# Kernel optimization log

Measured on AMD Instinct MI355X. Metric: run time of the kernel, lower is better.

The kernel has to match this reference:

```python
import jax, jax.numpy as jnp
import numpy as np

NHEAD = 16


def setup_inputs() -> dict:
    key = jax.random.key(0)
    ks = jax.random.split(key, 6)
    S, B, D = 2048, 2, 1024
    std = float(np.sqrt(6.0 / (D + D)))  # xavier_uniform bound
    inp = {
        "query": jax.random.normal(ks[0], (S, B, D), jnp.float32),
        "key": jax.random.normal(ks[1], (S, B, D), jnp.float32),
        "value": jax.random.normal(ks[2], (S, B, D), jnp.float32),
        "Wq": jax.random.uniform(ks[3], (D, D), jnp.float32, -std, std),
        "bq": jnp.ones((D,), jnp.float32),
        "Wk": jax.random.uniform(ks[4], (D, D), jnp.float32, -std, std),
        "bk": jnp.ones((D,), jnp.float32),
        "Wv": jax.random.uniform(ks[5], (D, D), jnp.float32, -std, std),
        "bv": jnp.ones((D,), jnp.float32),
    }
    return inp


def reference(query, key, value, Wq, bq, Wk, bk, Wv, bv):
    S, B, D = query.shape
    h = NHEAD
    d = D // h
    scale = jnp.asarray(d ** 0.5, query.dtype)
    # projections (nn.Linear: x @ W^T + b)
    q = (query @ Wq.T + bq).reshape(S, B, h, d)
    k = (key @ Wk.T + bk).reshape(S, B, h, d)
    v = (value @ Wv.T + bv).reshape(S, B, h, d)
    # batch_first=False path: scores [b,h,i,j], softmax over j, then AV
    scores = jnp.einsum('ibhd,jbhd->bhij', q, k) / scale
    attn = jax.nn.softmax(scores, axis=-1)
    out = jnp.einsum('bhij,jbhd->ibhd', attn, v).reshape(S, B, D)
    return out
```

## Files before the change

kernel.cpp:

```cpp
#include <hip/hip_runtime.h>
#include <hip/hip_bf16.h>

#define S_LEN 2048
#define BATCH 2
#define DMODEL 1024
#define NHEAD 16
#define HDIM 64
#define MTOT (S_LEN * BATCH)
#define QKV_ELEMS ((size_t)MTOT * DMODEL)
#define XOFF (3 * QKV_ELEMS)
#define WOFF (XOFF + 3 * QKV_ELEMS)
#define WSEG ((size_t)DMODEL * DMODEL)

typedef __bf16 bf16x8 __attribute__((ext_vector_type(8)));
typedef unsigned short u16x8 __attribute__((ext_vector_type(8)));
typedef float f32x4 __attribute__((ext_vector_type(4)));
typedef float f32x16 __attribute__((ext_vector_type(16)));
typedef unsigned int u32x4 __attribute__((ext_vector_type(4)));

__device__ __forceinline__ unsigned short f2bf(float f) {
    unsigned int u = __float_as_uint(f);
    u += 0x7FFFu + ((u >> 16) & 1u);
    return (unsigned short)(u >> 16);
}

__device__ __forceinline__ unsigned int pack2(float lo, float hi) {
    __hip_bfloat162 h = __float22bfloat162_rn(make_float2(lo, hi));
    unsigned int r;
    __builtin_memcpy(&r, &h, 4);
    return r;
}

__device__ __forceinline__ void gload_lds16(const void* g, void* l) {
    __builtin_amdgcn_global_load_lds(
        (const __attribute__((address_space(1))) unsigned int*)g,
        (__attribute__((address_space(3))) unsigned int*)l, 16, 0, 0);
}

__global__ __launch_bounds__(256) void cvt_kernel(
        const float* __restrict__ Xq, const float* __restrict__ Xk,
        const float* __restrict__ Xv, const float* __restrict__ Wq,
        const float* __restrict__ Wk, const float* __restrict__ Wv,
        unsigned short* __restrict__ ws)
{
    const int seg = blockIdx.y;
    const float* src;
    unsigned short* dst;
    int n4;
    if (seg < 3) {
        src = (seg == 0) ? Xq : (seg == 1) ? Xk : Xv;
        dst = ws + XOFF + (size_t)seg * QKV_ELEMS;
        n4  = (int)(QKV_ELEMS / 4);
    } else {
        const int s = seg - 3;
        src = (s == 0) ? Wq : (s == 1) ? Wk : Wv;
        dst = ws + WOFF + (size_t)s * WSEG;
        n4  = (int)(WSEG / 4);
    }
    const int stride = gridDim.x * blockDim.x;
    for (int i = blockIdx.x * blockDim.x + threadIdx.x; i < n4; i += stride) {
        const float4 v = ((const float4*)src)[i];
        uint2 o;
        o.x = pack2(v.x, v.y);
        o.y = pack2(v.z, v.w);
        ((uint2*)dst)[i] = o;
    }
}

#define PBM 128
#define PBN 128
#define PBK 32
#define QSCALE 0.18033688011112042f

__global__ __launch_bounds__(256, 3) void proj_kernel(
        const unsigned short* __restrict__ wsin,
        const float* __restrict__ bq, const float* __restrict__ bk,
        const float* __restrict__ bv, unsigned short* __restrict__ wsout)
{
    const int work = (blockIdx.x & 7) * 96 + (blockIdx.x >> 3);
    const int t    = work >> 8;
    const int rem  = work & 255;
    const int m0   = (rem >> 3) * PBM;
    const int n0   = (rem & 7) * PBN;

    const unsigned short* X = wsin + XOFF + (size_t)t * QKV_ELEMS;
    const unsigned short* W = wsin + WOFF + (size_t)t * WSEG;
    const float* bias = (t == 0) ? bq : (t == 1) ? bk : bv;
    unsigned short* out = wsout + (size_t)t * QKV_ELEMS;
    const float scale = (t == 0) ? QSCALE : 1.0f;

    __shared__ __align__(16) unsigned short Abuf[2][PBM * PBK];
    __shared__ __align__(16) unsigned short Bbuf[2][PBN * PBK];

    const int tid  = threadIdx.x;
    const int wave = tid >> 6;
    const int lane = tid & 63;
    const int lrow = lane & 15;
    const int lg   = lane >> 4;
    const int wr = (wave >> 1) * 64;
    const int wc = (wave & 1) * 64;

    f32x4 acc[4][4];
#pragma unroll
    for (int i = 0; i < 4; ++i)
#pragma unroll
        for (int j = 0; j < 4; ++j)
            acc[i][j] = (f32x4){0.f, 0.f, 0.f, 0.f};

    const int srow_ = tid >> 2;
    const int sc_   = tid & 3;
    const int gsw = (lg ^ (lrow & 3)) * 8;

#pragma unroll
    for (int i0 = 0; i0 < 2; ++i0) {
        const int row = i0 * 64 + srow_;
        const int c   = sc_ ^ (row & 3);
        gload_lds16(X + (size_t)(m0 + row) * DMODEL + c * 8, &Abuf[0][i0 * 2048 + tid * 8]);
        gload_lds16(W + (size_t)(n0 + row) * DMODEL + c * 8, &Bbuf[0][i0 * 2048 + tid * 8]);
    }
    __syncthreads();

    int cur = 0;
    for (int k0 = 0; k0 < DMODEL; k0 += PBK) {
        if (k0 + PBK < DMODEL) {
#pragma unroll
            for (int i0 = 0; i0 < 2; ++i0) {
                const int row = i0 * 64 + srow_;
                const int c   = sc_ ^ (row & 3);
                gload_lds16(X + (size_t)(m0 + row) * DMODEL + k0 + PBK + c * 8,
                            &Abuf[cur ^ 1][i0 * 2048 + tid * 8]);
                gload_lds16(W + (size_t)(n0 + row) * DMODEL + k0 + PBK + c * 8,
                            &Bbuf[cur ^ 1][i0 * 2048 + tid * 8]);
            }
        }

        bf16x8 af[4], bw[4];
#pragma unroll
        for (int i = 0; i < 4; ++i) {
            af[i] = *(const bf16x8*)&Abuf[cur][(wr + i * 16 + lrow) * PBK + gsw];
            bw[i] = *(const bf16x8*)&Bbuf[cur][(wc + i * 16 + lrow) * PBK + gsw];
        }
        __builtin_amdgcn_s_setprio(1);
#pragma unroll
        for (int i = 0; i < 4; ++i)
#pragma unroll
            for (int j = 0; j < 4; ++j)
                acc[i][j] = __builtin_amdgcn_mfma_f32_16x16x32_bf16(af[i], bw[j], acc[i][j], 0, 0, 0);
        __builtin_amdgcn_s_setprio(0);

        __syncthreads();
        cur ^= 1;
    }

#pragma unroll
    for (int j = 0; j < 4; ++j) {
        const int n  = n0 + wc + j * 16 + lrow;
        const float bv_ = bias[n];
        const int h  = n >> 6;
        const int dd = n & 63;
#pragma unroll
        for (int i = 0; i < 4; ++i) {
#pragma unroll
            for (int r = 0; r < 4; ++r) {
                const int m = m0 + wr + i * 16 + lg * 4 + r;
                const int s = m >> 1;
                const int b = m & 1;
                const float v = (acc[i][j][r] + bv_) * scale;
                size_t idx;
                if (t == 2)
                    idx = ((size_t)((b * NHEAD + h) * HDIM + dd)) * S_LEN + s;
                else
                    idx = ((size_t)((b * NHEAD + h) * S_LEN + s)) * HDIM + dd;
                out[idx] = f2bf(v);
            }
        }
    }
}

#define NP 32

__global__ __launch_bounds__(512, 4) void attn_kernel(
        const unsigned short* __restrict__ ws, float* __restrict__ out)
{
    const unsigned short* Qw = ws;
    const unsigned short* Kw = ws + QKV_ELEMS;
    const unsigned short* Vw = ws + 2 * QKV_ELEMS;

    const int bid = blockIdx.x;
    const int idx = bid >> 3;
    const int bh  = (bid & 7) * 4 + (idx >> 4);
    const int q0  = (idx & 15) * 128;

    __shared__ __align__(16) unsigned short SMEM[24576];
    unsigned short* Kb = SMEM;
    unsigned short* Vb = SMEM + 8192;
    unsigned int*   Pb = (unsigned int*)(SMEM + 16384);

    const int tid  = threadIdx.x;
    const int wave = tid >> 6;
    const int lane = tid & 63;
    const int l31  = lane & 31;
    const int half = lane >> 5;
    const int qsub = wave >> 1;
    const int pw   = wave & 1;

    const size_t base = (size_t)bh * S_LEN * HDIM;
    const int qrow = q0 + qsub * 32 + l31;

    bf16x8 qf[4];
#pragma unroll
    for (int c = 0; c < 4; ++c)
        qf[c] = *(const bf16x8*)(Qw + base + (size_t)qrow * HDIM + c * 16 + half * 8);

    bf16x8 ones;
    {
        u16x8 o;
#pragma unroll
        for (int e = 0; e < 8; ++e) o[e] = 0x3F80;
        ones = __builtin_bit_cast(bf16x8, o);
    }

    f32x16 Od0, Od1, Lacc;
#pragma unroll
    for (int i = 0; i < 16; ++i) { Od0[i] = 0.f; Od1[i] = 0.f; Lacc[i] = 0.f; }
    float mrun = -__builtin_inff();

    unsigned int* PuW = Pb + wave * 512;

    const int stile = tid >> 8;
    const int t256  = tid & 255;
    const int ksrow = t256 >> 3;
    const int ksg   = (t256 & 7) ^ (ksrow & 7);
    const int vrow  = t256 >> 2;
    const int vsg   = (t256 & 3) ^ ((vrow >> 1) & 3);

    int gk[4], gv[2];
#pragma unroll
    for (int c = 0; c < 4; ++c) gk[c] = ((c * 2 + half) ^ (l31 & 7)) * 8;
#pragma unroll
    for (int c = 0; c < 2; ++c) gv[c] = ((c * 2 + half) ^ ((l31 >> 1) & 3)) * 8;

    {
        const int tt = stile;
        gload_lds16(Kw + base + (size_t)(tt * 32 + ksrow) * HDIM + ksg * 8, &Kb[(tt & 3) * 2048 + t256 * 8]);
        gload_lds16(Vw + base + (size_t)vrow * S_LEN + tt * 32 + vsg * 8,   &Vb[(tt & 3) * 2048 + t256 * 8]);
    }
    __syncthreads();

    for (int p = 0; p < NP; ++p) {
        if (p < NP - 1) {
            const int tt = 2 * p + 2 + stile;
            gload_lds16(Kw + base + (size_t)(tt * 32 + ksrow) * HDIM + ksg * 8, &Kb[(tt & 3) * 2048 + t256 * 8]);
            gload_lds16(Vw + base + (size_t)vrow * S_LEN + tt * 32 + vsg * 8,   &Vb[(tt & 3) * 2048 + t256 * 8]);
        }

        const int tm = 2 * p + pw;
        const unsigned short* Klds = &Kb[(tm & 3) * 2048];
        const unsigned short* Vlds = &Vb[(tm & 3) * 2048];

        f32x16 S;
#pragma unroll
        for (int i = 0; i < 16; ++i) S[i] = 0.f;
        __builtin_amdgcn_s_setprio(1);
#pragma unroll
        for (int c = 0; c < 4; ++c) {
            const bf16x8 ka = *(const bf16x8*)&Klds[l31 * 64 + gk[c]];
            S = __builtin_amdgcn_mfma_f32_32x32x16_bf16(ka, qf[c], S, 0, 0, 0);
        }
        __builtin_amdgcn_s_setprio(0);

        float m8_[8];
#pragma unroll
        for (int i = 0; i < 8; ++i) m8_[i] = fmaxf(S[i], S[i + 8]);
        const float t0 = fmaxf(fmaxf(m8_[0], m8_[1]), m8_[2]);
        const float t1 = fmaxf(fmaxf(m8_[3], m8_[4]), m8_[5]);
        const float t2 = fmaxf(fmaxf(m8_[6], m8_[7]), t0);
        float mx = fmaxf(t1, t2);
        mx = fmaxf(mx, __shfl_xor(mx, 32, 64));

        if (!__all(mx - mrun <= 8.0f)) {
            const float mnew = fmaxf(mrun, mx);
            const float ex   = exp2f(mrun - mnew);
            mrun = mnew;
            Od0 *= ex;
            Od1 *= ex;
            Lacc *= ex;
        }

#pragma unroll
        for (int i = 0; i < 16; ++i) S[i] = exp2f(S[i] - mrun);

#pragma unroll
        for (int u = 0; u < 4; ++u) {
            uint2 two;
            two.x = pack2(S[4 * u],     S[4 * u + 1]);
            two.y = pack2(S[4 * u + 2], S[4 * u + 3]);
            *(uint2*)&PuW[(2 * u + half) * 64 + l31 * 2] = two;
        }
        __asm__ volatile("" ::: "memory");

        __builtin_amdgcn_s_setprio(1);
#pragma unroll
        for (int c = 0; c < 2; ++c) {
            const int row0 = 4 * c + 2 * half;
            const uint2 a = *(const uint2*)&PuW[row0 * 64 + l31 * 2];
            const uint2 b = *(const uint2*)&PuW[(row0 + 1) * 64 + l31 * 2];
            u32x4 pu; pu[0] = a.x; pu[1] = a.y; pu[2] = b.x; pu[3] = b.y;
            const bf16x8 pb = __builtin_bit_cast(bf16x8, pu);
            const bf16x8 va0 = *(const bf16x8*)&Vlds[l31 * 32 + gv[c]];
            const bf16x8 va1 = *(const bf16x8*)&Vlds[(32 + l31) * 32 + gv[c]];
            Od0  = __builtin_amdgcn_mfma_f32_32x32x16_bf16(va0,  pb, Od0,  0, 0, 0);
            Od1  = __builtin_amdgcn_mfma_f32_32x32x16_bf16(va1,  pb, Od1,  0, 0, 0);
            Lacc = __builtin_amdgcn_mfma_f32_32x32x16_bf16(ones, pb, Lacc, 0, 0, 0);
        }
        __builtin_amdgcn_s_setprio(0);

        __syncthreads();
    }

    float* mrg = (float*)SMEM;
    float* reg = mrg + qsub * 2176;
    if (pw) {
        reg[lane]      = mrun;
        reg[64 + lane] = Lacc[0];
#pragma unroll
        for (int i = 0; i < 16; ++i) {
            reg[128 + i * 64 + lane]        = Od0[i];
            reg[128 + (16 + i) * 64 + lane] = Od1[i];
        }
    }
    __syncthreads();
    if (!pw) {
        const float mb = reg[lane];
        const float lb = reg[64 + lane];
        const float ms = fmaxf(mrun, mb);
        const float sa = exp2f(mrun - ms);
        const float sb = exp2f(mb - ms);
        const float linv = 1.0f / (Lacc[0] * sa + lb * sb);

        const int bb = bh >> 4;
        const int hh = bh & 15;
        float* op = out + (size_t)qrow * (BATCH * DMODEL) + bb * DMODEL + hh * HDIM;
#pragma unroll
        for (int gg = 0; gg < 4; ++gg) {
            const int d0 = gg * 8 + half * 4;
            float4 v0, v1;
            v0.x = (Od0[gg * 4 + 0] * sa + reg[128 + (gg * 4 + 0) * 64 + lane] * sb) * linv;
            v0.y = (Od0[gg * 4 + 1] * sa + reg[128 + (gg * 4 + 1) * 64 + lane] * sb) * linv;
            v0.z = (Od0[gg * 4 + 2] * sa + reg[128 + (gg * 4 + 2) * 64 + lane] * sb) * linv;
            v0.w = (Od0[gg * 4 + 3] * sa + reg[128 + (gg * 4 + 3) * 64 + lane] * sb) * linv;
            v1.x = (Od1[gg * 4 + 0] * sa + reg[128 + (16 + gg * 4 + 0) * 64 + lane] * sb) * linv;
            v1.y = (Od1[gg * 4 + 1] * sa + reg[128 + (16 + gg * 4 + 1) * 64 + lane] * sb) * linv;
            v1.z = (Od1[gg * 4 + 2] * sa + reg[128 + (16 + gg * 4 + 2) * 64 + lane] * sb) * linv;
            v1.w = (Od1[gg * 4 + 3] * sa + reg[128 + (16 + gg * 4 + 3) * 64 + lane] * sb) * linv;
            *(float4*)(op + d0)      = v0;
            *(float4*)(op + 32 + d0) = v1;
        }
    }
}

extern "C" void kernel_launch(void* const* d_in, const int* in_sizes, int n_in,
                              void* d_out, int out_size, void* d_ws, size_t ws_size,
                              hipStream_t stream) {
    const float* q  = (const float*)d_in[0];
    const float* k  = (const float*)d_in[1];
    const float* v  = (const float*)d_in[2];
    const float* Wq = (const float*)d_in[3];
    const float* bq = (const float*)d_in[4];
    const float* Wk = (const float*)d_in[5];
    const float* bk = (const float*)d_in[6];
    const float* Wv = (const float*)d_in[7];
    const float* bv = (const float*)d_in[8];
    unsigned short* ws = (unsigned short*)d_ws;
    float* out = (float*)d_out;

    cvt_kernel<<<dim3(1024, 6), dim3(256), 0, stream>>>(q, k, v, Wq, Wk, Wv, ws);
    proj_kernel<<<dim3(768), dim3(256), 0, stream>>>(ws, bq, bk, bv, ws);
    attn_kernel<<<dim3(512), dim3(512), 0, stream>>>(ws, out);
}
```

Measured before the change: 133.6 us.

## Software-pipeline attention loop: overlap next QK^T MFMA with current softmax and PV

Restructures the flash-attention main loop into a software pipeline. The QK^T MFMAs for the next tile and the PV MFMAs for the previous tile are issued around the softmax of the current tile. The K/V LDS ring grows from 4 to 6 slots so a prefetch two periods ahead does not overwrite tiles still in use, and __syncthreads becomes an explicit vmcnt wait plus barrier. The aim is to hide the exp and softmax latency behind matrix-core work, at the cost of more LDS (which may lower occupancy) and more live registers. Only Lacc[0] is rescaled now, which relies on only element 0 being read later.

```diff
diff --git a/kernel.cpp b/kernel.cpp
--- a/kernel.cpp
+++ b/kernel.cpp
@@ -191,10 +191,10 @@
     const int bh  = (bid & 7) * 4 + (idx >> 4);
     const int q0  = (idx & 15) * 128;
 
-    __shared__ __align__(16) unsigned short SMEM[24576];
+    __shared__ __align__(16) unsigned short SMEM[32768];
     unsigned short* Kb = SMEM;
-    unsigned short* Vb = SMEM + 8192;
-    unsigned int*   Pb = (unsigned int*)(SMEM + 16384);
+    unsigned short* Vb = SMEM + 12288;
+    unsigned int*   Pb = (unsigned int*)(SMEM + 24576);
 
     const int tid  = threadIdx.x;
     const int wave = tid >> 6;
@@ -225,6 +225,8 @@
     for (int i = 0; i < 16; ++i) { Od0[i] = 0.f; Od1[i] = 0.f; Lacc[i] = 0.f; }
     float mrun = -__builtin_inff();
 
+    bf16x8 pb[2], va[4];
+
     unsigned int* PuW = Pb + wave * 512;
 
     const int stile = tid >> 8;
@@ -240,82 +242,128 @@
 #pragma unroll
     for (int c = 0; c < 2; ++c) gv[c] = ((c * 2 + half) ^ ((l31 >> 1) & 3)) * 8;
 
+#pragma unroll
+    for (int q = 0; q < 2; ++q) {
+        const int tt = 2 * q + stile;
+        gload_lds16(Kw + base + (size_t)(tt * 32 + ksrow) * HDIM + ksg * 8, &Kb[tt * 2048 + t256 * 8]);
+        gload_lds16(Vw + base + (size_t)vrow * S_LEN + tt * 32 + vsg * 8,   &Vb[tt * 2048 + t256 * 8]);
+    }
+    asm volatile("s_waitcnt vmcnt(0)" ::: "memory");
+    __builtin_amdgcn_s_barrier();
+
+    f32x16 Sa, Sb;
+
     {
-        const int tt = stile;
-        gload_lds16(Kw + base + (size_t)(tt * 32 + ksrow) * HDIM + ksg * 8, &Kb[(tt & 3) * 2048 + t256 * 8]);
-        gload_lds16(Vw + base + (size_t)vrow * S_LEN + tt * 32 + vsg * 8,   &Vb[(tt & 3) * 2048 + t256 * 8]);
-    }
-    __syncthreads();
-
-    for (int p = 0; p < NP; ++p) {
-        if (p < NP - 1) {
-            const int tt = 2 * p + 2 + stile;
-            gload_lds16(Kw + base + (size_t)(tt * 32 + ksrow) * HDIM + ksg * 8, &Kb[(tt & 3) * 2048 + t256 * 8]);
-            gload_lds16(Vw + base + (size_t)vrow * S_LEN + tt * 32 + vsg * 8,   &Vb[(tt & 3) * 2048 + t256 * 8]);
-        }
-
-        const int tm = 2 * p + pw;
-        const unsigned short* Klds = &Kb[(tm & 3) * 2048];
-        const unsigned short* Vlds = &Vb[(tm & 3) * 2048];
-
-        f32x16 S;
-#pragma unroll
-        for (int i = 0; i < 16; ++i) S[i] = 0.f;
+#pragma unroll
+        for (int i = 0; i < 16; ++i) Sa[i] = 0.f;
+        const unsigned short* Kl = &Kb[pw * 2048];
         __builtin_amdgcn_s_setprio(1);
 #pragma unroll
         for (int c = 0; c < 4; ++c) {
-            const bf16x8 ka = *(const bf16x8*)&Klds[l31 * 64 + gk[c]];
-            S = __builtin_amdgcn_mfma_f32_32x32x16_bf16(ka, qf[c], S, 0, 0, 0);
+            const bf16x8 ka = *(const bf16x8*)&Kl[l31 * 64 + gk[c]];
+            Sa = __builtin_amdgcn_mfma_f32_32x32x16_bf16(ka, qf[c], Sa, 0, 0, 0);
         }
         __builtin_amdgcn_s_setprio(0);
-
-        float m8_[8];
-#pragma unroll
-        for (int i = 0; i < 8; ++i) m8_[i] = fmaxf(S[i], S[i + 8]);
-        const float t0 = fmaxf(fmaxf(m8_[0], m8_[1]), m8_[2]);
-        const float t1 = fmaxf(fmaxf(m8_[3], m8_[4]), m8_[5]);
-        const float t2 = fmaxf(fmaxf(m8_[6], m8_[7]), t0);
-        float mx = fmaxf(t1, t2);
-        mx = fmaxf(mx, __shfl_xor(mx, 32, 64));
-
-        if (!__all(mx - mrun <= 8.0f)) {
-            const float mnew = fmaxf(mrun, mx);
-            const float ex   = exp2f(mrun - mnew);
-            mrun = mnew;
-            Od0 *= ex;
-            Od1 *= ex;
-            Lacc *= ex;
-        }
-
-#pragma unroll
-        for (int i = 0; i < 16; ++i) S[i] = exp2f(S[i] - mrun);
-
-#pragma unroll
-        for (int u = 0; u < 4; ++u) {
-            uint2 two;
-            two.x = pack2(S[4 * u],     S[4 * u + 1]);
-            two.y = pack2(S[4 * u + 2], S[4 * u + 3]);
-            *(uint2*)&PuW[(2 * u + half) * 64 + l31 * 2] = two;
-        }
-        __asm__ volatile("" ::: "memory");
-
+    }
+
+    int qsb = 2;
+    int csb = 0;
+
+    auto period = [&](f32x16& SCUR, f32x16& SNXT, const int p) {
+        if (p + 2 < NP) {
+            int ssb = qsb + 2; if (ssb >= 6) ssb -= 6;
+            const int tt = 2 * (p + 2) + stile;
+            gload_lds16(Kw + base + (size_t)(tt * 32 + ksrow) * HDIM + ksg * 8, &Kb[(ssb + stile) * 2048 + t256 * 8]);
+            gload_lds16(Vw + base + (size_t)vrow * S_LEN + tt * 32 + vsg * 8,   &Vb[(ssb + stile) * 2048 + t256 * 8]);
+        }
+        if (p + 1 < NP) {
+#pragma unroll
+            for (int i = 0; i < 16; ++i) SNXT[i] = 0.f;
+            const unsigned short* Kl = &Kb[(qsb + pw) * 2048];
+            __builtin_amdgcn_s_setprio(1);
+#pragma unroll
+            for (int c = 0; c < 4; ++c) {
+                const bf16x8 ka = *(const bf16x8*)&Kl[l31 * 64 + gk[c]];
+                SNXT = __builtin_amdgcn_mfma_f32_32x32x16_bf16(ka, qf[c], SNXT, 0, 0, 0);
+            }
+            __builtin_amdgcn_s_setprio(0);
+        }
+        if (p >= 1) {
+            __builtin_amdgcn_s_setprio(1);
+#pragma unroll
+            for (int c = 0; c < 2; ++c) {
+                Od0  = __builtin_amdgcn_mfma_f32_32x32x16_bf16(va[2 * c],     pb[c], Od0,  0, 0, 0);
+                Od1  = __builtin_amdgcn_mfma_f32_32x32x16_bf16(va[2 * c + 1], pb[c], Od1,  0, 0, 0);
+                Lacc = __builtin_amdgcn_mfma_f32_32x32x16_bf16(ones,          pb[c], Lacc, 0, 0, 0);
+            }
+            __builtin_amdgcn_s_setprio(0);
+        }
+        {
+            float m8_[8];
+#pragma unroll
+            for (int i = 0; i < 8; ++i) m8_[i] = fmaxf(SCUR[i], SCUR[i + 8]);
+            const float t0 = fmaxf(fmaxf(m8_[0], m8_[1]), m8_[2]);
+            const float t1 = fmaxf(fmaxf(m8_[3], m8_[4]), m8_[5]);
+            const float t2 = fmaxf(fmaxf(m8_[6], m8_[7]), t0);
+            float mx = fmaxf(t1, t2);
+            mx = fmaxf(mx, __shfl_xor(mx, 32, 64));
+
+            if (!__all(mx - mrun <= 8.0f)) {
+                const float mnew = fmaxf(mrun, mx);
+                const float ex   = exp2f(mrun - mnew);
+                mrun = mnew;
+                Od0 *= ex;
+                Od1 *= ex;
+                Lacc[0] *= ex;
+            }
+#pragma unroll
+            for (int i = 0; i < 16; ++i) SCUR[i] = exp2f(SCUR[i] - mrun);
+
+#pragma unroll
+            for (int u = 0; u < 4; ++u) {
+                uint2 two;
+                two.x = pack2(SCUR[4 * u],     SCUR[4 * u + 1]);
+                two.y = pack2(SCUR[4 * u + 2], SCUR[4 * u + 3]);
+                *(uint2*)&PuW[(2 * u + half) * 64 + l31 * 2] = two;
+            }
+            __asm__ volatile("" ::: "memory");
+        }
+        {
+#pragma unroll
+            for (int c = 0; c < 2; ++c) {
+                const int row0 = 4 * c + 2 * half;
+                const uint2 a = *(const uint2*)&PuW[row0 * 64 + l31 * 2];
+                const uint2 b = *(const uint2*)&PuW[(row0 + 1) * 64 + l31 * 2];
+                u32x4 pu; pu[0] = a.x; pu[1] = a.y; pu[2] = b.x; pu[3] = b.y;
+                pb[c] = __builtin_bit_cast(bf16x8, pu);
+            }
+            const unsigned short* Vl = &Vb[(csb + pw) * 2048];
+#pragma unroll
+            for (int c = 0; c < 2; ++c) {
+                va[2 * c]     = *(const bf16x8*)&Vl[l31 * 32 + gv[c]];
+                va[2 * c + 1] = *(const bf16x8*)&Vl[(32 + l31) * 32 + gv[c]];
+            }
+        }
+        asm volatile("s_waitcnt vmcnt(0)" ::: "memory");
+        __builtin_amdgcn_s_barrier();
+        qsb = (qsb >= 4) ? qsb - 4 : qsb + 2;
+        csb = (csb >= 4) ? csb - 4 : csb + 2;
+    };
+
+    for (int it = 0; it < NP / 2; ++it) {
+        period(Sa, Sb, 2 * it);
+        period(Sb, Sa, 2 * it + 1);
+    }
+
+    {
         __builtin_amdgcn_s_setprio(1);
 #pragma unroll
         for (int c = 0; c < 2; ++c) {
-            const int row0 = 4 * c + 2 * half;
-            const uint2 a = *(const uint2*)&PuW[row0 * 64 + l31 * 2];
-            const uint2 b = *(const uint2*)&PuW[(row0 + 1) * 64 + l31 * 2];
-            u32x4 pu; pu[0] = a.x; pu[1] = a.y; pu[2] = b.x; pu[3] = b.y;
-            const bf16x8 pb = __builtin_bit_cast(bf16x8, pu);
-            const bf16x8 va0 = *(const bf16x8*)&Vlds[l31 * 32 + gv[c]];
-            const bf16x8 va1 = *(const bf16x8*)&Vlds[(32 + l31) * 32 + gv[c]];
-            Od0  = __builtin_amdgcn_mfma_f32_32x32x16_bf16(va0,  pb, Od0,  0, 0, 0);
-            Od1  = __builtin_amdgcn_mfma_f32_32x32x16_bf16(va1,  pb, Od1,  0, 0, 0);
-            Lacc = __builtin_amdgcn_mfma_f32_32x32x16_bf16(ones, pb, Lacc, 0, 0, 0);
+            Od0  = __builtin_amdgcn_mfma_f32_32x32x16_bf16(va[2 * c],     pb[c], Od0,  0, 0, 0);
+            Od1  = __builtin_amdgcn_mfma_f32_32x32x16_bf16(va[2 * c + 1], pb[c], Od1,  0, 0, 0);
+            Lacc = __builtin_amdgcn_mfma_f32_32x32x16_bf16(ones,          pb[c], Lacc, 0, 0, 0);
         }
         __builtin_amdgcn_s_setprio(0);
-
-        __syncthreads();
     }
 
     float* mrg = (float*)SMEM;
```

Result: slower. 486.7 us (+264.5%).
